# Optimization experiments

Measured on AMD Instinct MI355X. Metric: run time of the kernel, lower is better.

Reference implementation:

```python
import jax, jax.numpy as jnp
from jax import lax
import numpy as np

T, B, I, H = 512, 512, 128, 128
EPS = 1e-4


def setup_inputs() -> dict:
    key = jax.random.key(0)
    ks = jax.random.split(key, 8)
    s = 1.0 / np.sqrt(H)
    x = jax.random.normal(ks[0], (T, B, I), dtype=jnp.float32)
    gt = jax.random.bernoulli(ks[1], 0.5, (T, B, 1)).astype(jnp.float32)
    W_ih = jax.random.uniform(ks[2], (3 * H, I), jnp.float32, -s, s)
    W_hh = jax.random.uniform(ks[3], (3 * H, H), jnp.float32, -s, s)
    b_ih = jax.random.uniform(ks[4], (3 * H,), jnp.float32, -s, s)
    b_hh = jax.random.uniform(ks[5], (3 * H,), jnp.float32, -s, s)
    W_dec = jax.random.uniform(ks[6], (1, H), jnp.float32, -s, s)
    b_dec = jax.random.uniform(ks[7], (1,), jnp.float32, -s, s)
    return {"x": x, "gt": gt, "W_ih": W_ih, "W_hh": W_hh, "b_ih": b_ih,
            "b_hh": b_hh, "W_dec": W_dec, "b_dec": b_dec}


def reference(x, gt, W_ih, W_hh, b_ih, b_hh, W_dec, b_dec):
    # Precompute input-side gate projections for all steps: [T, B, 3H]
    xp = jnp.einsum('tbi,gi->tbg', x, W_ih) + b_ih

    def step(carry, inp):
        h, acc = carry
        xpt, gtt = inp  # xpt: [B,3H], gtt: [B,1]
        hp = h @ W_hh.T + b_hh  # [B,3H]
        xr, xz, xn = jnp.split(xpt, 3, axis=-1)
        hr, hz, hn = jnp.split(hp, 3, axis=-1)
        r = jax.nn.sigmoid(xr + hr)
        z = jax.nn.sigmoid(xz + hz)
        n = jnp.tanh(xn + r * hn)
        h_new = (1.0 - z) * n + z * h
        C = jax.nn.sigmoid(h_new @ W_dec.T + b_dec)  # [B,1]
        nll = -jnp.sum(gtt * jnp.log(C + EPS) + (1.0 - gtt) * jnp.log(1.0 - C + EPS))
        return (h_new, acc + nll), None

    h0 = jnp.zeros((x.shape[1], W_hh.shape[1]), x.dtype)
    # loop t = 0 .. T-2: uses x[t] and gt[t+1]
    (_, nll), _ = lax.scan(step, (h0, jnp.zeros((), x.dtype)), (xp[:-1], gt[1:]))
    return nll / np.float32(gt.size)
```

## Files before the change

kernel.cpp:

```cpp
#include <hip/hip_runtime.h>
#include <stdint.h>

#define B_DIM 512
#define I_DIM 128
#define H_DIM 128
#define NSTEP 511

typedef __attribute__((ext_vector_type(4))) float f32x4;
typedef _Float16 half2_t __attribute__((ext_vector_type(2)));
typedef _Float16 half8_t __attribute__((ext_vector_type(8)));

#define BAR_LDS() asm volatile("s_waitcnt lgkmcnt(0)\n\ts_barrier" ::: "memory")
#define MFMA16(A, B, C) __builtin_amdgcn_mfma_f32_16x16x32_f16(A, B, C, 0, 0, 0)

__device__ __forceinline__ float frcp(float v) {
#if __has_builtin(__builtin_amdgcn_rcpf)
  return __builtin_amdgcn_rcpf(v);
#else
  return 1.f / v;
#endif
}
__device__ __forceinline__ unsigned pkrtz_u(float a, float b) {
#if __has_builtin(__builtin_amdgcn_cvt_pkrtz)
  return __builtin_bit_cast(unsigned, __builtin_amdgcn_cvt_pkrtz(a, b));
#else
  half2_t r; r.x = (_Float16)a; r.y = (_Float16)b;
  return __builtin_bit_cast(unsigned, r);
#endif
}

__global__ __launch_bounds__(1024, 4) void k_rec(
    const float* __restrict__ x, const float* __restrict__ gt,
    const float* __restrict__ Wih, const float* __restrict__ Whh,
    const float* __restrict__ bih, const float* __restrict__ bhh,
    const float* __restrict__ Wdec, const float* __restrict__ bdec,
    float* __restrict__ nll_part) {
  __shared__ __align__(16) _Float16 hT[2][16 * 128];
  __shared__ __align__(16) _Float16 xT[2][16 * 128];
  __shared__ __align__(16) float pp[2][3][4][128][4];
  __shared__ float gl[NSTEP * 16];

  const int tid = threadIdx.x;
  const int lane = tid & 63;
  const int w = tid >> 6;
  const int l15 = lane & 15, l4 = lane >> 4;
  const int row0 = blockIdx.x * 16;

#pragma unroll
  for (int q = 0; q < 8; ++q) {
    const int idx = tid + 1024 * q;
    if (idx < NSTEP * 16)
      gl[idx] = gt[(size_t)((idx >> 4) + 1) * B_DIM + row0 + (idx & 15)];
  }

  if (w < 8) {
    const int u = 16 * w + l15;

    half8_t bh[3][4];
#pragma unroll
    for (int g3 = 0; g3 < 3; ++g3)
#pragma unroll
      for (int ks = 0; ks < 4; ++ks) {
        const size_t off = (size_t)(g3 * H_DIM + u) * H_DIM + ks * 32 + l4 * 8;
        const float4 a = *(const float4*)(Whh + off);
        const float4 b = *(const float4*)(Whh + off + 4);
        half8_t v;
        v[0] = (_Float16)a.x; v[1] = (_Float16)a.y;
        v[2] = (_Float16)a.z; v[3] = (_Float16)a.w;
        v[4] = (_Float16)b.x; v[5] = (_Float16)b.y;
        v[6] = (_Float16)b.z; v[7] = (_Float16)b.w;
        bh[g3][ks] = v;
      }
    half8_t wdB[4];
#pragma unroll
    for (int ks = 0; ks < 4; ++ks) {
      half8_t v;
#pragma unroll
      for (int j = 0; j < 8; ++j)
        v[j] = (l15 == 0) ? (_Float16)Wdec[ks * 32 + l4 * 8 + j] : (_Float16)0.f;
      wdB[ks] = v;
    }
    const float bhn = bhh[2 * H_DIM + u];
    const float bd0 = bdec[0];
    const f32x4 cN = (f32x4){bhn, bhn, bhn, bhn};

    *(uint2*)((char*)hT[0] + tid * 8) = (uint2){0u, 0u};

    float h_old[4] = {0.f, 0.f, 0.f, 0.f};
    float nllA[4] = {0.f, 0.f, 0.f, 0.f};
    __syncthreads();
    __syncthreads();

#pragma unroll 1
    for (int i = 0; i < NSTEP; ++i) {
      const char* hb = (const char*)hT[i & 1];
      half8_t ah[4];
#pragma unroll
      for (int ks = 0; ks < 4; ++ks)
        ah[ks] = *(const half8_t*)(hb + l15 * 256 +
                                   ((((ks << 2) | l4) ^ l15) << 4));
      f32x4 aR = *(const f32x4*)&pp[i & 1][0][l4][u][0];
      f32x4 aZ = *(const f32x4*)&pp[i & 1][1][l4][u][0];
      const f32x4 pN = *(const f32x4*)&pp[i & 1][2][l4][u][0];
      f32x4 aN = cN;
#pragma unroll
      for (int ks = 0; ks < 4; ++ks) {
        aR = MFMA16(ah[ks], bh[0][ks], aR);
        aZ = MFMA16(ah[ks], bh[1][ks], aZ);
        aN = MFMA16(ah[ks], bh[2][ks], aN);
      }

      if (w == 0 && i > 0) {
        f32x4 aD = (f32x4){0.f, 0.f, 0.f, 0.f};
#pragma unroll
        for (int ks = 0; ks < 4; ++ks) aD = MFMA16(ah[ks], wdB[ks], aD);
        if (l15 == 0) {
#pragma unroll
          for (int r = 0; r < 4; ++r) {
            const float C = frcp(1.f + __expf(-(aD[r] + bd0)));
            const float g = gl[(i - 1) * 16 + 4 * l4 + r];
            nllA[r] -= g * __logf(C + 1e-4f) +
                       (1.f - g) * __logf(1.f - C + 1e-4f);
          }
        }
      }

      char* hw = (char*)hT[(i + 1) & 1];
#pragma unroll
      for (int r = 0; r < 4; ++r) {
        const float r_ = frcp(1.f + __expf(-aR[r]));
        const float z_ = frcp(1.f + __expf(-aZ[r]));
        const float a2 = pN[r] + r_ * aN[r];
        const float n_ = 1.f - 2.f * frcp(__expf(2.f * a2) + 1.f);
        const float hnew = n_ + z_ * (h_old[r] - n_);
        h_old[r] = hnew;
        const int b = 4 * l4 + r;
        *(_Float16*)(hw + b * 256 + (((u >> 3) ^ b) << 4) + (u & 7) * 2) =
            (_Float16)hnew;
      }
      BAR_LDS();
    }

    if (w == 0) {
      const char* hb = (const char*)hT[NSTEP & 1];
      half8_t ah[4];
#pragma unroll
      for (int ks = 0; ks < 4; ++ks)
        ah[ks] = *(const half8_t*)(hb + l15 * 256 +
                                   ((((ks << 2) | l4) ^ l15) << 4));
      f32x4 aD = (f32x4){0.f, 0.f, 0.f, 0.f};
#pragma unroll
      for (int ks = 0; ks < 4; ++ks) aD = MFMA16(ah[ks], wdB[ks], aD);
      if (l15 == 0) {
#pragma unroll
        for (int r = 0; r < 4; ++r) {
          const float C = frcp(1.f + __expf(-(aD[r] + bd0)));
          const float g = gl[(NSTEP - 1) * 16 + 4 * l4 + r];
          nllA[r] -= g * __logf(C + 1e-4f) +
                     (1.f - g) * __logf(1.f - C + 1e-4f);
          nll_part[row0 + 4 * l4 + r] = nllA[r];
        }
      }
    }
  } else {
    const int u = 16 * (w - 8) + l15;

    half8_t bx[3][4];
#pragma unroll
    for (int g3 = 0; g3 < 3; ++g3)
#pragma unroll
      for (int ks = 0; ks < 4; ++ks) {
        const size_t off = (size_t)(g3 * H_DIM + u) * H_DIM + ks * 32 + l4 * 8;
        const float4 a = *(const float4*)(Wih + off);
        const float4 b = *(const float4*)(Wih + off + 4);
        half8_t v;
        v[0] = (_Float16)a.x; v[1] = (_Float16)a.y;
        v[2] = (_Float16)a.z; v[3] = (_Float16)a.w;
        v[4] = (_Float16)b.x; v[5] = (_Float16)b.y;
        v[6] = (_Float16)b.z; v[7] = (_Float16)b.w;
        bx[g3][ks] = v;
      }
    const float brz0 = bih[u] + bhh[u];
    const float brz1 = bih[H_DIM + u] + bhh[H_DIM + u];
    const float bxn = bih[2 * H_DIM + u];
    const f32x4 cR = (f32x4){brz0, brz0, brz0, brz0};
    const f32x4 cZ = (f32x4){brz1, brz1, brz1, brz1};
    const f32x4 cXN = (f32x4){bxn, bxn, bxn, bxn};

    const int xt = tid - 512;
    const int sxr = xt >> 5, scq = xt & 31;
    const int sbyte = sxr * 256 + (((scq >> 1) ^ sxr) << 4) + (scq & 1) * 8;
    const size_t xlbase = ((size_t)row0 + sxr) * I_DIM + 4 * scq;

    {
      const float4 v0 = *(const float4*)&x[xlbase];
      const float4 v1 = *(const float4*)&x[(size_t)B_DIM * I_DIM + xlbase];
      uint2 p;
      p.x = pkrtz_u(v0.x, v0.y);
      p.y = pkrtz_u(v0.z, v0.w);
      *(uint2*)((char*)xT[0] + sbyte) = p;
      p.x = pkrtz_u(v1.x, v1.y);
      p.y = pkrtz_u(v1.z, v1.w);
      *(uint2*)((char*)xT[1] + sbyte) = p;
    }
    float4 xA = *(const float4*)&x[(size_t)2 * B_DIM * I_DIM + xlbase];
    __syncthreads();

    {
      const char* xb = (const char*)xT[0];
      half8_t af[4];
#pragma unroll
      for (int ks = 0; ks < 4; ++ks)
        af[ks] = *(const half8_t*)(xb + l15 * 256 +
                                   ((((ks << 2) | l4) ^ l15) << 4));
      f32x4 aR = cR, aZ = cZ, aN = cXN;
#pragma unroll
      for (int ks = 0; ks < 4; ++ks) {
        aR = MFMA16(af[ks], bx[0][ks], aR);
        aZ = MFMA16(af[ks], bx[1][ks], aZ);
        aN = MFMA16(af[ks], bx[2][ks], aN);
      }
      *(f32x4*)&pp[0][0][l4][u][0] = aR;
      *(f32x4*)&pp[0][1][l4][u][0] = aZ;
      *(f32x4*)&pp[0][2][l4][u][0] = aN;
    }
    __syncthreads();

#pragma unroll 1
    for (int i = 0; i < NSTEP; ++i) {
      const char* xb = (const char*)xT[(i + 1) & 1];
      half8_t af[4];
#pragma unroll
      for (int ks = 0; ks < 4; ++ks)
        af[ks] = *(const half8_t*)(xb + l15 * 256 +
                                   ((((ks << 2) | l4) ^ l15) << 4));
      f32x4 aR = cR, aZ = cZ, aN = cXN;
#pragma unroll
      for (int ks = 0; ks < 4; ++ks) {
        aR = MFMA16(af[ks], bx[0][ks], aR);
        aZ = MFMA16(af[ks], bx[1][ks], aZ);
        aN = MFMA16(af[ks], bx[2][ks], aN);
      }
      *(f32x4*)&pp[(i + 1) & 1][0][l4][u][0] = aR;
      *(f32x4*)&pp[(i + 1) & 1][1][l4][u][0] = aZ;
      *(f32x4*)&pp[(i + 1) & 1][2][l4][u][0] = aN;

      {
        uint2 p;
        p.x = pkrtz_u(xA.x, xA.y);
        p.y = pkrtz_u(xA.z, xA.w);
        *(uint2*)((char*)xT[i & 1] + sbyte) = p;
        const int nf = (i + 3 < 512) ? i + 3 : 511;
        xA = *(const float4*)&x[(size_t)nf * B_DIM * I_DIM + xlbase];
      }
      BAR_LDS();
    }
  }
}

__global__ __launch_bounds__(512) void k_fin(const float* __restrict__ nll_part,
                                             float* __restrict__ out) {
  __shared__ float red[8];
  const int tid = threadIdx.x;
  float v = nll_part[tid];
#pragma unroll
  for (int off = 32; off; off >>= 1) v += __shfl_down(v, off);
  if ((tid & 63) == 0) red[tid >> 6] = v;
  __syncthreads();
  if (tid == 0) {
    float s = 0.f;
#pragma unroll
    for (int i = 0; i < 8; ++i) s += red[i];
    out[0] = s * (1.f / (512.f * 512.f));
  }
}

extern "C" void kernel_launch(void* const* d_in, const int* in_sizes, int n_in,
                              void* d_out, int out_size, void* d_ws,
                              size_t ws_size, hipStream_t stream) {
  const float* x    = (const float*)d_in[0];
  const float* gt   = (const float*)d_in[1];
  const float* Wih  = (const float*)d_in[2];
  const float* Whh  = (const float*)d_in[3];
  const float* bih  = (const float*)d_in[4];
  const float* bhh  = (const float*)d_in[5];
  const float* Wdec = (const float*)d_in[6];
  const float* bdec = (const float*)d_in[7];

  float* nll_part = (float*)d_ws;

  k_rec<<<dim3(32), dim3(1024), 0, stream>>>(
      x, gt, Wih, Whh, bih, bhh, Wdec, bdec, nll_part);
  k_fin<<<dim3(1), dim3(512), 0, stream>>>(nll_part, (float*)d_out);
}
```

Measured before the change: 527.6 us.

## Halve input-projection waves and store gate preactivations as fp16 in LDS

```diff
diff --git a/kernel.cpp b/kernel.cpp
--- a/kernel.cpp
+++ b/kernel.cpp
@@ -28,8 +28,19 @@
   return __builtin_bit_cast(unsigned, r);
 #endif
 }
-
-__global__ __launch_bounds__(1024, 4) void k_rec(
+__device__ __forceinline__ uint2 pack_f32x4(f32x4 v) {
+  uint2 p;
+  p.x = pkrtz_u(v[0], v[1]);
+  p.y = pkrtz_u(v[2], v[3]);
+  return p;
+}
+__device__ __forceinline__ f32x4 unpack_u2(uint2 v) {
+  const half2_t a = __builtin_bit_cast(half2_t, v.x);
+  const half2_t b = __builtin_bit_cast(half2_t, v.y);
+  return (f32x4){(float)a.x, (float)a.y, (float)b.x, (float)b.y};
+}
+
+__global__ __launch_bounds__(768, 3) void k_rec(
     const float* __restrict__ x, const float* __restrict__ gt,
     const float* __restrict__ Wih, const float* __restrict__ Whh,
     const float* __restrict__ bih, const float* __restrict__ bhh,
@@ -37,7 +48,7 @@
     float* __restrict__ nll_part) {
   __shared__ __align__(16) _Float16 hT[2][16 * 128];
   __shared__ __align__(16) _Float16 xT[2][16 * 128];
-  __shared__ __align__(16) float pp[2][3][4][128][4];
+  __shared__ __align__(16) uint2 pp[2][3][4][128];
   __shared__ float gl[NSTEP * 16];
 
   const int tid = threadIdx.x;
@@ -47,8 +58,8 @@
   const int row0 = blockIdx.x * 16;
 
 #pragma unroll
-  for (int q = 0; q < 8; ++q) {
-    const int idx = tid + 1024 * q;
+  for (int q = 0; q < 11; ++q) {
+    const int idx = tid + 768 * q;
     if (idx < NSTEP * 16)
       gl[idx] = gt[(size_t)((idx >> 4) + 1) * B_DIM + row0 + (idx & 15)];
   }
@@ -99,9 +110,9 @@
       for (int ks = 0; ks < 4; ++ks)
         ah[ks] = *(const half8_t*)(hb + l15 * 256 +
                                    ((((ks << 2) | l4) ^ l15) << 4));
-      f32x4 aR = *(const f32x4*)&pp[i & 1][0][l4][u][0];
-      f32x4 aZ = *(const f32x4*)&pp[i & 1][1][l4][u][0];
-      const f32x4 pN = *(const f32x4*)&pp[i & 1][2][l4][u][0];
+      f32x4 aR = unpack_u2(pp[i & 1][0][l4][u]);
+      f32x4 aZ = unpack_u2(pp[i & 1][1][l4][u]);
+      const f32x4 pN = unpack_u2(pp[i & 1][2][l4][u]);
       f32x4 aN = cN;
 #pragma unroll
       for (int ks = 0; ks < 4; ++ks) {
@@ -163,47 +174,56 @@
       }
     }
   } else {
-    const int u = 16 * (w - 8) + l15;
-
-    half8_t bx[3][4];
-#pragma unroll
-    for (int g3 = 0; g3 < 3; ++g3)
-#pragma unroll
-      for (int ks = 0; ks < 4; ++ks) {
-        const size_t off = (size_t)(g3 * H_DIM + u) * H_DIM + ks * 32 + l4 * 8;
-        const float4 a = *(const float4*)(Wih + off);
-        const float4 b = *(const float4*)(Wih + off + 4);
-        half8_t v;
-        v[0] = (_Float16)a.x; v[1] = (_Float16)a.y;
-        v[2] = (_Float16)a.z; v[3] = (_Float16)a.w;
-        v[4] = (_Float16)b.x; v[5] = (_Float16)b.y;
-        v[6] = (_Float16)b.z; v[7] = (_Float16)b.w;
-        bx[g3][ks] = v;
-      }
-    const float brz0 = bih[u] + bhh[u];
-    const float brz1 = bih[H_DIM + u] + bhh[H_DIM + u];
-    const float bxn = bih[2 * H_DIM + u];
-    const f32x4 cR = (f32x4){brz0, brz0, brz0, brz0};
-    const f32x4 cZ = (f32x4){brz1, brz1, brz1, brz1};
-    const f32x4 cXN = (f32x4){bxn, bxn, bxn, bxn};
+    const int wx = w - 8;
+    const int u0 = 32 * wx + l15;
+
+    half8_t bx[2][3][4];
+    float brz0[2], brz1[2], bxn[2];
+#pragma unroll
+    for (int c = 0; c < 2; ++c) {
+      const int u = u0 + 16 * c;
+#pragma unroll
+      for (int g3 = 0; g3 < 3; ++g3)
+#pragma unroll
+        for (int ks = 0; ks < 4; ++ks) {
+          const size_t off =
+              (size_t)(g3 * H_DIM + u) * H_DIM + ks * 32 + l4 * 8;
+          const float4 a = *(const float4*)(Wih + off);
+          const float4 b = *(const float4*)(Wih + off + 4);
+          half8_t v;
+          v[0] = (_Float16)a.x; v[1] = (_Float16)a.y;
+          v[2] = (_Float16)a.z; v[3] = (_Float16)a.w;
+          v[4] = (_Float16)b.x; v[5] = (_Float16)b.y;
+          v[6] = (_Float16)b.z; v[7] = (_Float16)b.w;
+          bx[c][g3][ks] = v;
+        }
+      brz0[c] = bih[u] + bhh[u];
+      brz1[c] = bih[H_DIM + u] + bhh[H_DIM + u];
+      bxn[c] = bih[2 * H_DIM + u];
+    }
 
     const int xt = tid - 512;
-    const int sxr = xt >> 5, scq = xt & 31;
-    const int sbyte = sxr * 256 + (((scq >> 1) ^ sxr) << 4) + (scq & 1) * 8;
-    const size_t xlbase = ((size_t)row0 + sxr) * I_DIM + 4 * scq;
+    const int sxr = xt >> 4;
+    const int c16 = xt & 15;
+    const int sbyte = sxr * 256 + ((c16 ^ sxr) << 4);
+    const size_t xlbase = ((size_t)row0 + sxr) * I_DIM + c16 * 8;
 
     {
-      const float4 v0 = *(const float4*)&x[xlbase];
-      const float4 v1 = *(const float4*)&x[(size_t)B_DIM * I_DIM + xlbase];
-      uint2 p;
-      p.x = pkrtz_u(v0.x, v0.y);
-      p.y = pkrtz_u(v0.z, v0.w);
-      *(uint2*)((char*)xT[0] + sbyte) = p;
-      p.x = pkrtz_u(v1.x, v1.y);
-      p.y = pkrtz_u(v1.z, v1.w);
-      *(uint2*)((char*)xT[1] + sbyte) = p;
-    }
-    float4 xA = *(const float4*)&x[(size_t)2 * B_DIM * I_DIM + xlbase];
+#pragma unroll
+      for (int t = 0; t < 2; ++t) {
+        const float4 v0 = *(const float4*)&x[(size_t)t * B_DIM * I_DIM + xlbase];
+        const float4 v1 =
+            *(const float4*)&x[(size_t)t * B_DIM * I_DIM + xlbase + 4];
+        uint4 p;
+        p.x = pkrtz_u(v0.x, v0.y);
+        p.y = pkrtz_u(v0.z, v0.w);
+        p.z = pkrtz_u(v1.x, v1.y);
+        p.w = pkrtz_u(v1.z, v1.w);
+        *(uint4*)((char*)xT[t] + sbyte) = p;
+      }
+    }
+    float4 xA0 = *(const float4*)&x[(size_t)2 * B_DIM * I_DIM + xlbase];
+    float4 xA1 = *(const float4*)&x[(size_t)2 * B_DIM * I_DIM + xlbase + 4];
     __syncthreads();
 
     {
@@ -213,16 +233,21 @@
       for (int ks = 0; ks < 4; ++ks)
         af[ks] = *(const half8_t*)(xb + l15 * 256 +
                                    ((((ks << 2) | l4) ^ l15) << 4));
-      f32x4 aR = cR, aZ = cZ, aN = cXN;
-#pragma unroll
-      for (int ks = 0; ks < 4; ++ks) {
-        aR = MFMA16(af[ks], bx[0][ks], aR);
-        aZ = MFMA16(af[ks], bx[1][ks], aZ);
-        aN = MFMA16(af[ks], bx[2][ks], aN);
-      }
-      *(f32x4*)&pp[0][0][l4][u][0] = aR;
-      *(f32x4*)&pp[0][1][l4][u][0] = aZ;
-      *(f32x4*)&pp[0][2][l4][u][0] = aN;
+#pragma unroll
+      for (int c = 0; c < 2; ++c) {
+        f32x4 aR = (f32x4){brz0[c], brz0[c], brz0[c], brz0[c]};
+        f32x4 aZ = (f32x4){brz1[c], brz1[c], brz1[c], brz1[c]};
+        f32x4 aN = (f32x4){bxn[c], bxn[c], bxn[c], bxn[c]};
+#pragma unroll
+        for (int ks = 0; ks < 4; ++ks) {
+          aR = MFMA16(af[ks], bx[c][0][ks], aR);
+          aZ = MFMA16(af[ks], bx[c][1][ks], aZ);
+          aN = MFMA16(af[ks], bx[c][2][ks], aN);
+        }
+        pp[0][0][l4][u0 + 16 * c] = pack_f32x4(aR);
+        pp[0][1][l4][u0 + 16 * c] = pack_f32x4(aZ);
+        pp[0][2][l4][u0 + 16 * c] = pack_f32x4(aN);
+      }
     }
     __syncthreads();
 
@@ -234,24 +259,33 @@
       for (int ks = 0; ks < 4; ++ks)
         af[ks] = *(const half8_t*)(xb + l15 * 256 +
                                    ((((ks << 2) | l4) ^ l15) << 4));
-      f32x4 aR = cR, aZ = cZ, aN = cXN;
-#pragma unroll
-      for (int ks = 0; ks < 4; ++ks) {
-        aR = MFMA16(af[ks], bx[0][ks], aR);
-        aZ = MFMA16(af[ks], bx[1][ks], aZ);
-        aN = MFMA16(af[ks], bx[2][ks], aN);
-      }
-      *(f32x4*)&pp[(i + 1) & 1][0][l4][u][0] = aR;
-      *(f32x4*)&pp[(i + 1) & 1][1][l4][u][0] = aZ;
-      *(f32x4*)&pp[(i + 1) & 1][2][l4][u][0] = aN;
+#pragma unroll
+      for (int c = 0; c < 2; ++c) {
+        f32x4 aR = (f32x4){brz0[c], brz0[c], brz0[c], brz0[c]};
+        f32x4 aZ = (f32x4){brz1[c], brz1[c], brz1[c], brz1[c]};
+        f32x4 aN = (f32x4){bxn[c], bxn[c], bxn[c], bxn[c]};
+#pragma unroll
+        for (int ks = 0; ks < 4; ++ks) {
+          aR = MFMA16(af[ks], bx[c][0][ks], aR);
+          aZ = MFMA16(af[ks], bx[c][1][ks], aZ);
+          aN = MFMA16(af[ks], bx[c][2][ks], aN);
+        }
+        pp[(i + 1) & 1][0][l4][u0 + 16 * c] = pack_f32x4(aR);
+        pp[(i + 1) & 1][1][l4][u0 + 16 * c] = pack_f32x4(aZ);
+        pp[(i + 1) & 1][2][l4][u0 + 16 * c] = pack_f32x4(aN);
+      }
 
       {
-        uint2 p;
-        p.x = pkrtz_u(xA.x, xA.y);
-        p.y = pkrtz_u(xA.z, xA.w);
-        *(uint2*)((char*)xT[i & 1] + sbyte) = p;
-        const int nf = (i + 3 < 512) ? i + 3 : 511;
-        xA = *(const float4*)&x[(size_t)nf * B_DIM * I_DIM + xlbase];
+        uint4 p;
+        p.x = pkrtz_u(xA0.x, xA0.y);
+        p.y = pkrtz_u(xA0.z, xA0.w);
+        p.z = pkrtz_u(xA1.x, xA1.y);
+        p.w = pkrtz_u(xA1.z, xA1.w);
+        *(uint4*)((char*)xT[i & 1] + sbyte) = p;
+        const size_t trow =
+            (size_t)((i + 3 < 512) ? i + 3 : 511) * B_DIM * I_DIM;
+        xA0 = *(const float4*)&x[trow + xlbase];
+        xA1 = *(const float4*)&x[trow + xlbase + 4];
       }
       BAR_LDS();
     }
@@ -289,7 +323,7 @@
 
   float* nll_part = (float*)d_ws;
 
-  k_rec<<<dim3(32), dim3(1024), 0, stream>>>(
+  k_rec<<<dim3(32), dim3(768), 0, stream>>>(
       x, gt, Wih, Whh, bih, bhh, Wdec, bdec, nll_part);
   k_fin<<<dim3(1), dim3(512), 0, stream>>>(nll_part, (float*)d_out);
 }
```

New measurement: 519.3 us. No clear change (-1.6%).
